# Optimization experiments

Measured on AMD Instinct MI355X. Metric: run time of the kernel, lower is better.

The kernel has to match this reference:

```python
import jax, jax.numpy as jnp
import numpy as np

NUM_LOCAL = 100000
NUM_EDGES = 1600000
IN_C = 128
OUT_C = 128
NUM_OWNED = 80000


def setup_inputs() -> dict:
    key = jax.random.key(0)
    k1, k2, k3, k4, k5 = jax.random.split(key, 5)
    x = jax.random.normal(k1, (NUM_LOCAL, IN_C), dtype=jnp.float32)
    weight = jax.random.normal(k2, (IN_C, OUT_C), dtype=jnp.float32) * (1.0 / np.sqrt(IN_C))
    bias = jnp.zeros((OUT_C,), dtype=jnp.float32)
    # D^{-1/2} is positive; uniform in (0, 1]
    deg_inv_sqrt = jax.random.uniform(k3, (NUM_LOCAL,), dtype=jnp.float32, minval=0.05, maxval=1.0)
    row = jax.random.randint(k4, (NUM_EDGES,), 0, NUM_LOCAL, dtype=jnp.int32)  # dst
    col = jax.random.randint(k5, (NUM_EDGES,), 0, NUM_LOCAL, dtype=jnp.int32)  # src
    return {"x": x, "weight": weight, "bias": bias, "deg_inv_sqrt": deg_inv_sqrt,
            "row": row, "col": col, "num_owned": NUM_OWNED}


def reference(x, weight, bias, deg_inv_sqrt, row, col, num_owned):
    # h = (x @ W) scaled by D^{-1/2}
    h = x @ weight                                   # [N_local, out_c]
    h = deg_inv_sqrt[:, None] * h
    # SpMM: out[i] = sum_{(src->i) in E} h[src]
    msgs = h[col]                                    # gather [E, out_c]
    agg = jax.ops.segment_sum(msgs, row, num_segments=NUM_LOCAL)
    # keep owned nodes only, rescale by D^{-1/2}
    out = agg[:num_owned] * deg_inv_sqrt[:num_owned, None]
    return out + bias
```

## Files before the change

### kernel.cpp

```cpp
#include <hip/hip_runtime.h>

typedef unsigned int uint32;
typedef short bf16x8 __attribute__((ext_vector_type(8)));
typedef float f32x4 __attribute__((ext_vector_type(4)));

#define NSB 256
#define MAXNB 1280
#define C_SLOT 1536
#define SMEM_BYTES 34816

__device__ __forceinline__ unsigned short f2bf(float f) {
  uint32 b = __float_as_uint(f);
  uint32 r = (b + 0x7fffu + ((b >> 16) & 1u)) >> 16;
  return (unsigned short)r;
}
__device__ __forceinline__ float bf2f(unsigned short u) {
  return __uint_as_float(((uint32)u) << 16);
}

__device__ __forceinline__
void gemm_tile(char* smem, int row0, const float* __restrict__ x,
               const short* __restrict__ wtb, const float* __restrict__ dis,
               unsigned short* __restrict__ hb, int NL) {
  short* Bt = (short*)smem;
  const int tid  = threadIdx.x;
  const int lane = tid & 63;
  const int wid  = tid >> 6;
  const int li   = lane & 15;
  const int lh   = lane >> 4;

  {
    const uint4* src = (const uint4*)wtb;
    for (int u = tid; u < 2048; u += 256) {
      int c = u >> 4, j = u & 15;
      *(uint4*)&Bt[c * 136 + j * 8] = src[u];
    }
  }
  __syncthreads();

  f32x4 acc[2][8] = {};

#pragma unroll
  for (int kh = 0; kh < 2; ++kh) {
#pragma unroll
    for (int c = 0; c < 2; ++c) {
      const int kkg = kh * 64 + c * 32 + lh * 8;
      bf16x8 af[2], bfr[8];
#pragma unroll
      for (int rf = 0; rf < 2; ++rf) {
        int gr = row0 + wid * 32 + rf * 16 + li;
        union { bf16x8 v; ushort4 q[2]; } t;
        if (gr < NL) {
          const float* xp = &x[(size_t)gr * 128 + kkg];
          float4 v0 = *(const float4*)xp;
          float4 v1 = *(const float4*)(xp + 4);
          t.q[0] = make_ushort4(f2bf(v0.x), f2bf(v0.y), f2bf(v0.z), f2bf(v0.w));
          t.q[1] = make_ushort4(f2bf(v1.x), f2bf(v1.y), f2bf(v1.z), f2bf(v1.w));
        } else {
          t.q[0] = make_ushort4(0, 0, 0, 0);
          t.q[1] = make_ushort4(0, 0, 0, 0);
        }
        af[rf] = t.v;
      }
#pragma unroll
      for (int cf = 0; cf < 8; ++cf)
        bfr[cf] = *(const bf16x8*)&Bt[(cf * 16 + li) * 136 + kkg];
#pragma unroll
      for (int rf = 0; rf < 2; ++rf)
#pragma unroll
        for (int cf = 0; cf < 8; ++cf)
          acc[rf][cf] = __builtin_amdgcn_mfma_f32_16x16x32_bf16(af[rf], bfr[cf], acc[rf][cf], 0, 0, 0);
    }
  }

#pragma unroll
  for (int rf = 0; rf < 2; ++rf) {
#pragma unroll
    for (int j = 0; j < 4; ++j) {
      int r = row0 + wid * 32 + rf * 16 + lh * 4 + j;
      if (r < NL) {
        float d = dis[r];
        size_t base = (size_t)r * 128 + li;
#pragma unroll
        for (int cf = 0; cf < 8; ++cf)
          hb[base + cf * 16] = f2bf(acc[rf][cf][j] * d);
      }
    }
  }
}

__global__ __launch_bounds__(256)
void stage1_kernel(const float* __restrict__ w, short* __restrict__ wtb,
                   int* __restrict__ gcur, int NB) {
  int i = blockIdx.x * 256 + threadIdx.x;
  if (i < 128 * 128) {
    int c = i >> 7, k = i & 127;
    wtb[c * 128 + k] = (short)f2bf(w[(size_t)k * 128 + c]);
  }
  if (i < NB) gcur[i] = i * C_SLOT;
}

__global__ __launch_bounds__(256)
void stage2_kernel(const int* __restrict__ row, const int* __restrict__ col,
                   int* __restrict__ gcur, uint32* __restrict__ pairs,
                   int NE, int num_owned, int NB, int chunk, int scatBlocks,
                   const float* __restrict__ x, const short* __restrict__ wtb,
                   const float* __restrict__ dis, unsigned short* __restrict__ hb, int NL) {
  __shared__ char smem[SMEM_BYTES];
  const int tid = threadIdx.x;

  if ((int)blockIdx.x < scatBlocks) {
    int* h    = (int*)smem;
    int* base = h + MAXNB;
    const int blk = blockIdx.x;
    for (int b = tid; b < NB; b += 256) h[b] = 0;
    __syncthreads();
    int s = blk * chunk;
    int e = min(s + chunk, NE);
    for (int i = s + tid; i < e; i += 256) {
      int r = row[i];
      if (r < num_owned) atomicAdd(&h[r >> 6], 1);
    }
    __syncthreads();
    for (int b = tid; b < NB; b += 256) {
      int c = h[b];
      base[b] = (c > 0) ? atomicAdd(&gcur[b], c) : 0;
    }
    __syncthreads();
    for (int b = tid; b < NB; b += 256) h[b] = 0;
    __syncthreads();
    for (int i = s + tid; i < e; i += 256) {
      int r = row[i];
      if (r < num_owned) {
        int b = r >> 6;
        int off = atomicAdd(&h[b], 1);
        int p = base[b] + off;
        if (p < (b + 1) * C_SLOT)
          pairs[p] = ((uint32)col[i] << 6) | (uint32)(r & 63);
      }
    }
    return;
  }

  gemm_tile(smem, (int)(blockIdx.x - scatBlocks) * 128, x, wtb, dis, hb, NL);
}

__global__ __launch_bounds__(256)
void stage3_kernel(const uint32* __restrict__ pairs, const int* __restrict__ gcur,
                   int* __restrict__ csr, int* __restrict__ nstart, int* __restrict__ nend,
                   int num_owned, int NB, int gemmRowOffBlocks,
                   const float* __restrict__ x, const short* __restrict__ wtb,
                   const float* __restrict__ dis, unsigned short* __restrict__ hb, int NL) {
  __shared__ char smem[SMEM_BYTES];
  const int tid = threadIdx.x;

  if ((int)blockIdx.x < NB) {
    int* h    = (int*)smem;
    int* offs = h + 64;
    int* cur  = offs + 64;
    const int b = blockIdx.x;
    if (tid < 64) { h[tid] = 0; cur[tid] = 0; }
    __syncthreads();
    const int bs = b * C_SLOT;
    const int be = min(gcur[b], bs + C_SLOT);
    for (int e = bs + tid; e < be; e += 256)
      atomicAdd(&h[pairs[e] & 63u], 1);
    __syncthreads();
    if (tid < 64) {
      int v = h[tid];
      int s = v;
#pragma unroll
      for (int off = 1; off < 64; off <<= 1) {
        int t = __shfl_up(s, off, 64);
        if (tid >= off) s += t;
      }
      offs[tid] = s - v;
      int node = b * 64 + tid;
      if (node < num_owned) {
        nstart[node] = bs + s - v;
        nend[node]   = bs + s;
      }
    }
    __syncthreads();
    for (int e = bs + tid; e < be; e += 256) {
      uint32 p = pairs[e];
      int nl = (int)(p & 63u);
      int pos = atomicAdd(&cur[nl], 1);
      csr[bs + offs[nl] + pos] = (int)(p >> 6);
    }
    return;
  }

  gemm_tile(smem, (gemmRowOffBlocks + (int)blockIdx.x - NB) * 128, x, wtb, dis, hb, NL);
}

__global__ __launch_bounds__(256)
void agg_kernel(const unsigned short* __restrict__ hb, const int* __restrict__ csr,
                const int* __restrict__ nstart, const int* __restrict__ nend,
                const float* __restrict__ dis, const float* __restrict__ bias,
                float* __restrict__ out, int num_owned) {
  int node = blockIdx.x * 4 + (threadIdx.x >> 6);
  int lane = threadIdx.x & 63;
  if (node >= num_owned) return;
  const int g  = lane >> 4;
  const int i8 = (lane & 15) * 8;
  int ns = nstart[node], ne = nend[node];
  int cnt = ne - ns;
  float a[8] = {};

  auto acc16 = [&](uint4 v) {
    a[0] += bf2f((unsigned short)(v.x & 0xffff));
    a[1] += bf2f((unsigned short)(v.x >> 16));
    a[2] += bf2f((unsigned short)(v.y & 0xffff));
    a[3] += bf2f((unsigned short)(v.y >> 16));
    a[4] += bf2f((unsigned short)(v.z & 0xffff));
    a[5] += bf2f((unsigned short)(v.z >> 16));
    a[6] += bf2f((unsigned short)(v.w & 0xffff));
    a[7] += bf2f((unsigned short)(v.w >> 16));
  };

  int myidx = (lane < cnt) ? csr[ns + lane] : 0;
  int m = cnt < 64 ? cnt : 64;
  int T = (m + 15) >> 4;
  for (int t = 0; t < T; ++t) {
    int p0 = t * 16 + g;
    int p1 = p0 + 4, p2 = p0 + 8, p3 = p0 + 12;
    int s0 = __shfl(myidx, p0 < m ? p0 : 0, 64);
    int s1 = __shfl(myidx, p1 < m ? p1 : 0, 64);
    int s2 = __shfl(myidx, p2 < m ? p2 : 0, 64);
    int s3 = __shfl(myidx, p3 < m ? p3 : 0, 64);
    uint4 v0 = *(const uint4*)&hb[(size_t)s0 * 128 + i8];
    uint4 v1 = *(const uint4*)&hb[(size_t)s1 * 128 + i8];
    uint4 v2 = *(const uint4*)&hb[(size_t)s2 * 128 + i8];
    uint4 v3 = *(const uint4*)&hb[(size_t)s3 * 128 + i8];
    if (p0 < m) acc16(v0);
    if (p1 < m) acc16(v1);
    if (p2 < m) acc16(v2);
    if (p3 < m) acc16(v3);
  }
  for (int e = ns + 64 + g; e < ne; e += 4) {
    int s = csr[e];
    uint4 v = *(const uint4*)&hb[(size_t)s * 128 + i8];
    acc16(v);
  }

#pragma unroll
  for (int k = 0; k < 8; ++k) {
    a[k] += __shfl_xor(a[k], 16, 64);
    a[k] += __shfl_xor(a[k], 32, 64);
  }
  if (g == 0) {
    float d = dis[node];
    float4 b0 = *(const float4*)&bias[i8];
    float4 b1 = *(const float4*)&bias[i8 + 4];
    float4 o0, o1;
    o0.x = a[0] * d + b0.x; o0.y = a[1] * d + b0.y;
    o0.z = a[2] * d + b0.z; o0.w = a[3] * d + b0.w;
    o1.x = a[4] * d + b1.x; o1.y = a[5] * d + b1.y;
    o1.z = a[6] * d + b1.z; o1.w = a[7] * d + b1.w;
    *(float4*)&out[(size_t)node * 128 + i8] = o0;
    *(float4*)&out[(size_t)node * 128 + i8 + 4] = o1;
  }
}

extern "C" void kernel_launch(void* const* d_in, const int* in_sizes, int n_in,
                              void* d_out, int out_size, void* d_ws, size_t ws_size,
                              hipStream_t stream) {
  const float* x    = (const float*)d_in[0];
  const float* w    = (const float*)d_in[1];
  const float* bias = (const float*)d_in[2];
  const float* dis  = (const float*)d_in[3];
  const int*   row  = (const int*)d_in[4];
  const int*   col  = (const int*)d_in[5];

  const int OC = in_sizes[2];
  const int IC = in_sizes[1] / OC;
  const int NL = in_sizes[0] / IC;
  const int NE = in_sizes[4];
  const int num_owned = out_size / OC;
  float* out = (float*)d_out;

  const int NB = (num_owned + 63) >> 6;
  const int chunk = (((NE + NSB - 1) / NSB) + 255) & ~255;

  char* ws = (char*)d_ws;
  size_t off = 0;
  auto alloc = [&](size_t bytes) -> void* {
    void* p = ws + off;
    off += (bytes + 255) & ~(size_t)255;
    return p;
  };
  unsigned short* hb  = (unsigned short*)alloc((size_t)NL * OC * sizeof(unsigned short));
  short*  wtb    = (short*)alloc((size_t)IC * OC * sizeof(short));
  int*    gcur   = (int*)alloc((size_t)NB * sizeof(int));
  uint32* pairs  = (uint32*)alloc((size_t)NB * C_SLOT * sizeof(uint32));
  int*    csr    = (int*)alloc((size_t)NB * C_SLOT * sizeof(int));
  int*    nstart = (int*)alloc((size_t)num_owned * sizeof(int));
  int*    nend   = (int*)alloc((size_t)num_owned * sizeof(int));
  (void)ws_size; (void)n_in;

  const int gemmBlocks = (NL + 127) / 128;
  const int gB = gemmBlocks / 2;
  const int gC = gemmBlocks - gB;

  stage1_kernel<<<64, 256, 0, stream>>>(w, wtb, gcur, NB);

  stage2_kernel<<<NSB + gB, 256, 0, stream>>>(row, col, gcur, pairs,
                                              NE, num_owned, NB, chunk, NSB,
                                              x, wtb, dis, hb, NL);

  stage3_kernel<<<NB + gC, 256, 0, stream>>>(pairs, gcur, csr, nstart, nend,
                                             num_owned, NB, gB,
                                             x, wtb, dis, hb, NL);

  agg_kernel<<<(num_owned + 3) / 4, 256, 0, stream>>>(hb, csr, nstart, nend, dis, bias, out, num_owned);
}
```

Measured before the change: 111.4 us.

## Move all GEMM tiles into stage2 and make stage3 a lean CSR kernel

All GEMM tiles now run in stage2 alongside the edge-scatter blocks, where before they were split half and half between stage2 and stage3. Stage3 becomes a pure per-bucket CSR build with only small static shared arrays, which should give it higher occupancy and shorter blocks. The trade-off is that stage2 gets longer, and the CSR build no longer overlaps any GEMM work. Whether this helps depends on how the GEMM, scatter and CSR work balance against each other.

```diff
diff --git a/kernel.cpp b/kernel.cpp
--- a/kernel.cpp
+++ b/kernel.cpp
@@ -103,13 +103,13 @@
 __global__ __launch_bounds__(256)
 void stage2_kernel(const int* __restrict__ row, const int* __restrict__ col,
                    int* __restrict__ gcur, uint32* __restrict__ pairs,
-                   int NE, int num_owned, int NB, int chunk, int scatBlocks,
+                   int NE, int num_owned, int NB, int chunk,
                    const float* __restrict__ x, const short* __restrict__ wtb,
                    const float* __restrict__ dis, unsigned short* __restrict__ hb, int NL) {
   __shared__ char smem[SMEM_BYTES];
   const int tid = threadIdx.x;
 
-  if ((int)blockIdx.x < scatBlocks) {
+  if ((int)blockIdx.x < NSB) {
     int* h    = (int*)smem;
     int* base = h + MAXNB;
     const int blk = blockIdx.x;
@@ -142,56 +142,47 @@
     return;
   }
 
-  gemm_tile(smem, (int)(blockIdx.x - scatBlocks) * 128, x, wtb, dis, hb, NL);
+  gemm_tile(smem, (int)(blockIdx.x - NSB) * 128, x, wtb, dis, hb, NL);
 }
 
 __global__ __launch_bounds__(256)
 void stage3_kernel(const uint32* __restrict__ pairs, const int* __restrict__ gcur,
                    int* __restrict__ csr, int* __restrict__ nstart, int* __restrict__ nend,
-                   int num_owned, int NB, int gemmRowOffBlocks,
-                   const float* __restrict__ x, const short* __restrict__ wtb,
-                   const float* __restrict__ dis, unsigned short* __restrict__ hb, int NL) {
-  __shared__ char smem[SMEM_BYTES];
+                   int num_owned) {
+  __shared__ int h[64];
+  __shared__ int offs[64];
+  __shared__ int cur[64];
   const int tid = threadIdx.x;
-
-  if ((int)blockIdx.x < NB) {
-    int* h    = (int*)smem;
-    int* offs = h + 64;
-    int* cur  = offs + 64;
-    const int b = blockIdx.x;
-    if (tid < 64) { h[tid] = 0; cur[tid] = 0; }
-    __syncthreads();
-    const int bs = b * C_SLOT;
-    const int be = min(gcur[b], bs + C_SLOT);
-    for (int e = bs + tid; e < be; e += 256)
-      atomicAdd(&h[pairs[e] & 63u], 1);
-    __syncthreads();
-    if (tid < 64) {
-      int v = h[tid];
-      int s = v;
-#pragma unroll
-      for (int off = 1; off < 64; off <<= 1) {
-        int t = __shfl_up(s, off, 64);
-        if (tid >= off) s += t;
-      }
-      offs[tid] = s - v;
-      int node = b * 64 + tid;
-      if (node < num_owned) {
-        nstart[node] = bs + s - v;
-        nend[node]   = bs + s;
-      }
-    }
-    __syncthreads();
-    for (int e = bs + tid; e < be; e += 256) {
-      uint32 p = pairs[e];
-      int nl = (int)(p & 63u);
-      int pos = atomicAdd(&cur[nl], 1);
-      csr[bs + offs[nl] + pos] = (int)(p >> 6);
-    }
-    return;
-  }
-
-  gemm_tile(smem, (gemmRowOffBlocks + (int)blockIdx.x - NB) * 128, x, wtb, dis, hb, NL);
+  const int b = blockIdx.x;
+  if (tid < 64) { h[tid] = 0; cur[tid] = 0; }
+  __syncthreads();
+  const int bs = b * C_SLOT;
+  const int be = min(gcur[b], bs + C_SLOT);
+  for (int e = bs + tid; e < be; e += 256)
+    atomicAdd(&h[pairs[e] & 63u], 1);
+  __syncthreads();
+  if (tid < 64) {
+    int v = h[tid];
+    int s = v;
+#pragma unroll
+    for (int off = 1; off < 64; off <<= 1) {
+      int t = __shfl_up(s, off, 64);
+      if (tid >= off) s += t;
+    }
+    offs[tid] = s - v;
+    int node = b * 64 + tid;
+    if (node < num_owned) {
+      nstart[node] = bs + s - v;
+      nend[node]   = bs + s;
+    }
+  }
+  __syncthreads();
+  for (int e = bs + tid; e < be; e += 256) {
+    uint32 p = pairs[e];
+    int nl = (int)(p & 63u);
+    int pos = atomicAdd(&cur[nl], 1);
+    csr[bs + offs[nl] + pos] = (int)(p >> 6);
+  }
 }
 
 __global__ __launch_bounds__(256)
@@ -300,18 +291,14 @@
   (void)ws_size; (void)n_in;
 
   const int gemmBlocks = (NL + 127) / 128;
-  const int gB = gemmBlocks / 2;
-  const int gC = gemmBlocks - gB;
 
   stage1_kernel<<<64, 256, 0, stream>>>(w, wtb, gcur, NB);
 
-  stage2_kernel<<<NSB + gB, 256, 0, stream>>>(row, col, gcur, pairs,
-                                              NE, num_owned, NB, chunk, NSB,
-                                              x, wtb, dis, hb, NL);
-
-  stage3_kernel<<<NB + gC, 256, 0, stream>>>(pairs, gcur, csr, nstart, nend,
-                                             num_owned, NB, gB,
-                                             x, wtb, dis, hb, NL);
+  stage2_kernel<<<NSB + gemmBlocks, 256, 0, stream>>>(row, col, gcur, pairs,
+                                                      NE, num_owned, NB, chunk,
+                                                      x, wtb, dis, hb, NL);
+
+  stage3_kernel<<<NB, 256, 0, stream>>>(pairs, gcur, csr, nstart, nend, num_owned);
 
   agg_kernel<<<(num_owned + 3) / 4, 256, 0, stream>>>(hb, csr, nstart, nend, dis, bias, out, num_owned);
 }
```

Result: faster. 103.4 us (-7.3%).
